# Kernel tuning notes

Hardware: AMD Instinct MI355X
Metric: run time of the kernel (lower is better)

## Reference

```python
import jax, jax.numpy as jnp
import numpy as np

DIM = 1024
HEADS = 16
HEAD_DIM = DIM // HEADS
MLP = 4 * DIM
EPS = 1e-5


def layer_norm(x, g, b):
    mu = jnp.mean(x, axis=-1, keepdims=True)
    var = jnp.var(x, axis=-1, keepdims=True)
    return (x - mu) * jax.lax.rsqrt(var + EPS) * g + b


def rope_cos_sin(n, d):
    inv_freq = 1.0 / (10000.0 ** (jnp.arange(0, d, 2, dtype=jnp.float32) / d))
    t = jnp.arange(n, dtype=jnp.float32)
    freqs = jnp.outer(t, inv_freq)          # [N, d/2]
    emb = jnp.concatenate([freqs, freqs], -1)  # [N, d]
    return jnp.cos(emb), jnp.sin(emb)


def rotate_half(x):
    x1, x2 = x[..., ::2], x[..., 1::2]
    return jnp.concatenate([-x2, x1], axis=-1)


def setup_inputs() -> dict:
    key = jax.random.key(0)
    ks = jax.random.split(key, 16)
    B, N = 2, 2048
    s = lambda fan_in: 1.0 / np.sqrt(fan_in)
    inp = {
        "x": jax.random.normal(ks[0], (B, N, DIM), jnp.float32),
        "t_emb": jax.random.normal(ks[1], (B, DIM), jnp.float32),
        "norm1_g": jnp.ones((DIM,), jnp.float32),
        "norm1_b": jnp.zeros((DIM,), jnp.float32),
        "Wq": jax.random.normal(ks[2], (DIM, DIM), jnp.float32) * s(DIM),
        "Wk": jax.random.normal(ks[3], (DIM, DIM), jnp.float32) * s(DIM),
        "Wv": jax.random.normal(ks[4], (DIM, DIM), jnp.float32) * s(DIM),
        "Wo": jax.random.normal(ks[5], (DIM, DIM), jnp.float32) * s(DIM),
        "norm2_g": jnp.ones((DIM,), jnp.float32),
        "norm2_b": jnp.zeros((DIM,), jnp.float32),
        "W1": jax.random.normal(ks[6], (DIM, MLP), jnp.float32) * s(DIM),
        "W2": jax.random.normal(ks[7], (MLP, DIM), jnp.float32) * s(MLP),
        "ada_W": jax.random.normal(ks[8], (DIM, 6 * DIM), jnp.float32) * s(DIM),
        "ada_b": jnp.zeros((6 * DIM,), jnp.float32),
    }
    return inp


def reference(x, t_emb, norm1_g, norm1_b, Wq, Wk, Wv, Wo,
              norm2_g, norm2_b, W1, W2, ada_W, ada_b):
    B, N, C = x.shape
    H, D = HEADS, HEAD_DIM
    scale = D ** -0.5

    mod = jax.nn.silu(t_emb) @ ada_W + ada_b          # [B, 6C]
    (shift_msa, scale_msa, gate_msa,
     shift_mlp, scale_mlp, gate_mlp) = jnp.split(mod, 6, axis=-1)

    xn = layer_norm(x, norm1_g, norm1_b) * (1 + scale_msa[:, None, :]) + shift_msa[:, None, :]

    q = (xn @ Wq).reshape(B, N, H, D).transpose(0, 2, 1, 3)  # [B,H,N,D]
    k = (xn @ Wk).reshape(B, N, H, D).transpose(0, 2, 1, 3)
    v = (xn @ Wv).reshape(B, N, H, D).transpose(0, 2, 1, 3)

    cos, sin = rope_cos_sin(N, D)                     # [N, D]
    q = q * cos + rotate_half(q) * sin
    k = k * cos + rotate_half(k) * sin

    attn = jnp.einsum('bhnd,bhmd->bhnm', q, k) * scale  # explicit O(N^2) scores
    attn = jax.nn.softmax(attn, axis=-1)
    out = jnp.einsum('bhnm,bhmd->bhnd', attn, v)

    out = out.transpose(0, 2, 1, 3).reshape(B, N, C) @ Wo
    x = x + gate_msa[:, None, :] * out

    xn = layer_norm(x, norm2_g, norm2_b) * (1 + scale_mlp[:, None, :]) + shift_mlp[:, None, :]
    mlp = jax.nn.gelu(xn @ W1, approximate=False) @ W2
    x = x + gate_mlp[:, None, :] * mlp
    return x
```

## Files before the change

kernel.cpp:

```cpp
#include <hip/hip_runtime.h>
#include <math.h>

#define BB    2
#define NN    2048
#define CDIM  1024
#define HEADS 16
#define HDIM  64
#define MLPD  4096
#define MODC  6144
#define EPSV  1e-5f
#define LOG2E 1.4426950408889634f
#define MSPLIT 16

typedef __attribute__((ext_vector_type(8))) short s8v;
typedef __attribute__((ext_vector_type(4))) float f4v;

__device__ inline unsigned short f2bf(float f) {
  union { float f; unsigned u; } v; v.f = f;
  unsigned r = v.u + 0x7FFFu + ((v.u >> 16) & 1u);
  return (unsigned short)(r >> 16);
}
__device__ inline float bf2f(unsigned short h) {
  union { unsigned u; float f; } v; v.u = ((unsigned)h) << 16;
  return v.f;
}

template<int CTRL>
__device__ __forceinline__ float dpp_max_step(float v) {
  int iv = __float_as_int(v);
  int sh = __builtin_amdgcn_update_dpp(iv, iv, CTRL, 0xF, 0xF, false);
  return fmaxf(v, __int_as_float(sh));
}
__device__ __forceinline__ float max16(float v) {
  v = dpp_max_step<0xB1>(v);
  v = dpp_max_step<0x4E>(v);
  v = dpp_max_step<0x124>(v);
  v = dpp_max_step<0x128>(v);
  return v;
}

__global__ __launch_bounds__(256) void mod_part(
    const float* __restrict__ t_emb, const float* __restrict__ ada_W,
    float* __restrict__ part) {
  int j = blockIdx.x * 256 + threadIdx.x;
  int b = blockIdx.y, ks = blockIdx.z;
  __shared__ float st[64];
  if (threadIdx.x < 64) {
    float v = t_emb[b * CDIM + ks * 64 + threadIdx.x];
    st[threadIdx.x] = v / (1.0f + expf(-v));
  }
  __syncthreads();
  float acc = 0.f;
  const float* wp = ada_W + (size_t)(ks * 64) * MODC + j;
  #pragma unroll 8
  for (int i = 0; i < 64; ++i) acc += st[i] * wp[(size_t)i * MODC];
  part[((size_t)ks * BB + b) * MODC + j] = acc;
}

__global__ __launch_bounds__(256) void mod_reduce(
    const float* __restrict__ part, const float* __restrict__ ada_b,
    float* __restrict__ mod) {
  int idx = blockIdx.x * 256 + threadIdx.x;
  int b = idx / MODC, j = idx % MODC;
  float a = ada_b[j];
  #pragma unroll
  for (int s = 0; s < MSPLIT; ++s) a += part[((size_t)s * BB + b) * MODC + j];
  mod[(size_t)b * MODC + j] = a;
}

__device__ inline float wave_sum64(float v) {
  for (int o = 32; o > 0; o >>= 1) v += __shfl_down(v, o, 64);
  return v;
}

__global__ __launch_bounds__(256) void ln_mod_bf16(
    const float* __restrict__ x, const float* __restrict__ g,
    const float* __restrict__ bta, const float* __restrict__ mod,
    int shift_off, int scale_off, unsigned short* __restrict__ out) {
  int r = blockIdx.x;
  int b = r / NN;
  int t = threadIdx.x;
  const float* xr = x + (size_t)r * CDIM;
  float4 xv = ((const float4*)xr)[t];
  float s  = xv.x + xv.y + xv.z + xv.w;
  float s2 = xv.x*xv.x + xv.y*xv.y + xv.z*xv.z + xv.w*xv.w;
  __shared__ float ws1[4], ws2[4];
  float sw = wave_sum64(s), s2w = wave_sum64(s2);
  int lane = t & 63, wid = t >> 6;
  if (lane == 0) { ws1[wid] = sw; ws2[wid] = s2w; }
  __syncthreads();
  float mu  = (ws1[0] + ws1[1] + ws1[2] + ws1[3]) * (1.0f / CDIM);
  float var = (ws2[0] + ws2[1] + ws2[2] + ws2[3]) * (1.0f / CDIM) - mu * mu;
  float rstd = rsqrtf(var + EPSV);
  const float* mods = mod + (size_t)b * MODC;
  float4 gv = ((const float4*)g)[t];
  float4 bv = ((const float4*)bta)[t];
  float4 sc = ((const float4*)(mods + scale_off))[t];
  float4 sh = ((const float4*)(mods + shift_off))[t];
  ushort4 ov;
  ov.x = f2bf(((xv.x - mu) * rstd * gv.x + bv.x) * (1.0f + sc.x) + sh.x);
  ov.y = f2bf(((xv.y - mu) * rstd * gv.y + bv.y) * (1.0f + sc.y) + sh.y);
  ov.z = f2bf(((xv.z - mu) * rstd * gv.z + bv.z) * (1.0f + sc.z) + sh.z);
  ov.w = f2bf(((xv.w - mu) * rstd * gv.w + bv.w) * (1.0f + sc.w) + sh.w);
  ((ushort4*)(out + (size_t)r * CDIM))[t] = ov;
}

__global__ __launch_bounds__(256) void wcast_all(
    const float* __restrict__ Wq, const float* __restrict__ Wk,
    const float* __restrict__ Wv, const float* __restrict__ Wo,
    const float* __restrict__ W1, const float* __restrict__ W2,
    unsigned short* __restrict__ Wqkvt, unsigned short* __restrict__ Wot,
    unsigned short* __restrict__ W1t, unsigned short* __restrict__ W2t) {
  int bid = blockIdx.x;
  const float* W; unsigned short* Wt; int K, N, t;
  if (bid < 4096) {
    int m = bid >> 10;
    t = bid & 1023;
    K = CDIM; N = CDIM;
    W  = (m == 0) ? Wq : (m == 1) ? Wk : (m == 2) ? Wv : Wo;
    Wt = (m == 3) ? Wot : (Wqkvt + (size_t)m * CDIM * CDIM);
  } else if (bid < 8192) {
    t = bid - 4096; K = CDIM; N = MLPD; W = W1; Wt = W1t;
  } else {
    t = bid - 8192; K = MLPD; N = CDIM; W = W2; Wt = W2t;
  }
  int ntiles = N >> 5;
  int n0 = (t % ntiles) * 32, k0 = (t / ntiles) * 32;
  __shared__ float tile[32][33];
  int tx = threadIdx.x & 31, ty = threadIdx.x >> 5;
  #pragma unroll
  for (int p = 0; p < 4; ++p)
    tile[ty + p * 8][tx] = W[(size_t)(k0 + ty + p * 8) * N + n0 + tx];
  __syncthreads();
  #pragma unroll
  for (int p = 0; p < 4; ++p)
    Wt[(size_t)(n0 + ty + p * 8) * K + k0 + tx] = f2bf(tile[tx][ty + p * 8]);
}

__global__ __launch_bounds__(1024) void mfma_gemm_big(
    const unsigned short* __restrict__ A,
    const unsigned short* __restrict__ Bt,
    int M, int N, int K,
    unsigned short* __restrict__ Ob, unsigned short* __restrict__ Ob2,
    unsigned short* __restrict__ Ob3, int mode) {
  __shared__ unsigned short SH[3 * 16384];
  int tid = threadIdx.x;
  int wave = tid >> 6, lane = tid & 63;
  int quad = lane >> 4, l15 = lane & 15;
  int m0 = blockIdx.y * 128, n0 = blockIdx.x * 128;
  int pos = wave & 7;
  int om = pos >> 1, on = pos & 1;
  int ks = wave >> 3;

  f4v acc[2][4] = {};

  int srow = lane >> 3;
  int ksrc = ((lane & 7) ^ (lane >> 3)) << 3;
  const int nt = K >> 6;

  #define STAGE_BIG(T, BUF)                                                    \
    {                                                                          \
      int k0_ = (T) << 6;                                                      \
      unsigned short* dsta = SH + (BUF) * 16384 + wave * 512;                  \
      const unsigned short* ga =                                               \
          A + (size_t)(m0 + 8 * wave + srow) * K + k0_ + ksrc;                 \
      __builtin_amdgcn_global_load_lds(                                        \
          (const __attribute__((address_space(1))) unsigned int*)(const void*)ga, \
          (__attribute__((address_space(3))) unsigned int*)(void*)dsta,        \
          16, 0, 0);                                                           \
      const unsigned short* gb =                                               \
          Bt + (size_t)(n0 + 8 * wave + srow) * K + k0_ + ksrc;                \
      __builtin_amdgcn_global_load_lds(                                        \
          (const __attribute__((address_space(1))) unsigned int*)(const void*)gb, \
          (__attribute__((address_space(3))) unsigned int*)(void*)(dsta + 8192), \
          16, 0, 0);                                                           \
    }

  STAGE_BIG(0, 0);
  STAGE_BIG(1, 1);
  asm volatile("s_waitcnt vmcnt(2)" ::: "memory");
  __syncthreads();

  int kx = (ks * 32 + quad * 8) ^ ((l15 & 7) << 3);

  int rbuf = 0, sbuf = 2;
  for (int t = 0; t < nt; ++t) {
    if (t + 2 < nt) STAGE_BIG(t + 2, sbuf);

    const unsigned short* base = SH + rbuf * 16384;
    s8v af[2], bf[4];
    #pragma unroll
    for (int i = 0; i < 2; ++i)
      af[i] = *(const s8v*)(base + (om * 32 + i * 16 + l15) * 64 + kx);
    #pragma unroll
    for (int j = 0; j < 4; ++j)
      bf[j] = *(const s8v*)(base + 8192 + (on * 64 + j * 16 + l15) * 64 + kx);
    #pragma unroll
    for (int i = 0; i < 2; ++i)
      #pragma unroll
      for (int j = 0; j < 4; ++j)
        acc[i][j] = __builtin_amdgcn_mfma_f32_16x16x32_bf16(
            af[i], bf[j], acc[i][j], 0, 0, 0);

    if (t + 2 < nt) {
      asm volatile("s_waitcnt vmcnt(2)" ::: "memory");
    } else if (t + 1 < nt) {
      asm volatile("s_waitcnt vmcnt(0)" ::: "memory");
    }
    __syncthreads();
    rbuf = (rbuf == 2) ? 0 : rbuf + 1;
    sbuf = (sbuf == 2) ? 0 : sbuf + 1;
  }
  #undef STAGE_BIG

  float* red = (float*)SH;
  if (wave >= 8) {
    int rb = (wave - 8) * 2304 + lane * 36;
    #pragma unroll
    for (int i = 0; i < 2; ++i)
      #pragma unroll
      for (int j = 0; j < 4; ++j)
        *(f4v*)(red + rb + (i * 4 + j) * 4) = acc[i][j];
  }
  __syncthreads();
  if (wave < 8) {
    int rb = wave * 2304 + lane * 36;
    #pragma unroll
    for (int i = 0; i < 2; ++i)
      #pragma unroll
      for (int j = 0; j < 4; ++j)
        acc[i][j] += *(const f4v*)(red + rb + (i * 4 + j) * 4);
    #pragma unroll
    for (int i = 0; i < 2; ++i) {
      int rbase = m0 + om * 32 + i * 16 + quad * 4;
      #pragma unroll
      for (int j = 0; j < 4; ++j) {
        int c = n0 + on * 64 + j * 16 + l15;
        #pragma unroll
        for (int rg = 0; rg < 4; ++rg) {
          int r = rbase + rg;
          float v = acc[i][j][rg];
          if (mode == 0) {
            unsigned short* dst = (c < 1024) ? Ob : ((c < 2048) ? Ob2 : Ob3);
            dst[(size_t)r * 1024 + (c & 1023)] = f2bf(v);
          } else {
            v = 0.5f * v * (1.0f + erff(v * 0.70710678118f));
            Ob[(size_t)r * N + c] = f2bf(v);
          }
        }
      }
    }
  }
}

__global__ __launch_bounds__(1024) void mfma_gemm_res(
    const unsigned short* __restrict__ A,
    const unsigned short* __restrict__ Bt,
    int M, int N, int K,
    float* __restrict__ O0,
    const float* __restrict__ res, const float* __restrict__ mod,
    int gate_off) {
  __shared__ unsigned short SH[3 * 16384];
  int tid = threadIdx.x;
  int wave = tid >> 6, lane = tid & 63;
  int quad = lane >> 4, l15 = lane & 15;
  int m0 = blockIdx.y * 128, n0 = blockIdx.x * 128;
  int pos = wave & 7;
  int om = pos >> 1, on = pos & 1;
  int ks = wave >> 3;

  f4v acc[2][4] = {};

  int srow = lane >> 3;
  int ksrc = ((lane & 7) ^ (lane >> 3)) << 3;
  const int nt = K >> 6;

  #define STAGE_RES(T, BUF)                                                    \
    {                                                                          \
      int k0_ = (T) << 6;                                                      \
      unsigned short* dsta = SH + (BUF) * 16384 + wave * 512;                  \
      const unsigned short* ga =                                               \
          A + (size_t)(m0 + 8 * wave + srow) * K + k0_ + ksrc;                 \
      __builtin_amdgcn_global_load_lds(                                        \
          (const __attribute__((address_space(1))) unsigned int*)(const void*)ga, \
          (__attribute__((address_space(3))) unsigned int*)(void*)dsta,        \
          16, 0, 0);                                                           \
      const unsigned short* gb =                                               \
          Bt + (size_t)(n0 + 8 * wave + srow) * K + k0_ + ksrc;                \
      __builtin_amdgcn_global_load_lds(                                        \
          (const __attribute__((address_space(1))) unsigned int*)(const void*)gb, \
          (__attribute__((address_space(3))) unsigned int*)(void*)(dsta + 8192), \
          16, 0, 0);                                                           \
    }

  STAGE_RES(0, 0);
  STAGE_RES(1, 1);
  asm volatile("s_waitcnt vmcnt(2)" ::: "memory");
  __syncthreads();

  int kx = (ks * 32 + quad * 8) ^ ((l15 & 7) << 3);

  int rbuf = 0, sbuf = 2;
  for (int t = 0; t < nt; ++t) {
    if (t + 2 < nt) STAGE_RES(t + 2, sbuf);

    const unsigned short* base = SH + rbuf * 16384;
    s8v af[2], bf[4];
    #pragma unroll
    for (int i = 0; i < 2; ++i)
      af[i] = *(const s8v*)(base + (om * 32 + i * 16 + l15) * 64 + kx);
    #pragma unroll
    for (int j = 0; j < 4; ++j)
      bf[j] = *(const s8v*)(base + 8192 + (on * 64 + j * 16 + l15) * 64 + kx);
    #pragma unroll
    for (int i = 0; i < 2; ++i)
      #pragma unroll
      for (int j = 0; j < 4; ++j)
        acc[i][j] = __builtin_amdgcn_mfma_f32_16x16x32_bf16(
            af[i], bf[j], acc[i][j], 0, 0, 0);

    if (t + 2 < nt) {
      asm volatile("s_waitcnt vmcnt(2)" ::: "memory");
    } else if (t + 1 < nt) {
      asm volatile("s_waitcnt vmcnt(0)" ::: "memory");
    }
    __syncthreads();
    rbuf = (rbuf == 2) ? 0 : rbuf + 1;
    sbuf = (sbuf == 2) ? 0 : sbuf + 1;
  }
  #undef STAGE_RES

  float* red = (float*)SH;
  if (wave >= 8) {
    int rb = (wave - 8) * 2304 + lane * 36;
    #pragma unroll
    for (int i = 0; i < 2; ++i)
      #pragma unroll
      for (int j = 0; j < 4; ++j)
        *(f4v*)(red + rb + (i * 4 + j) * 4) = acc[i][j];
  }
  __syncthreads();
  if (wave < 8) {
    int rb = wave * 2304 + lane * 36;
    #pragma unroll
    for (int i = 0; i < 2; ++i)
      #pragma unroll
      for (int j = 0; j < 4; ++j)
        acc[i][j] += *(const f4v*)(red + rb + (i * 4 + j) * 4);
    #pragma unroll
    for (int i = 0; i < 2; ++i) {
      int rbase = m0 + om * 32 + i * 16 + quad * 4;
      #pragma unroll
      for (int j = 0; j < 4; ++j) {
        int c = n0 + on * 64 + j * 16 + l15;
        #pragma unroll
        for (int rg = 0; rg < 4; ++rg) {
          int r = rbase + rg;
          int bb2 = r >> 11;
          O0[(size_t)r * N + c] =
              res[(size_t)r * N + c] + mod[bb2 * MODC + gate_off + c] * acc[i][j][rg];
        }
      }
    }
  }
}

__global__ __launch_bounds__(256) void rope_qk(
    unsigned short* __restrict__ qb, const unsigned short* __restrict__ kb,
    unsigned short* __restrict__ kpack, float qscale) {
  int r = blockIdx.x;
  int b = r / NN, n = r % NN;
  int t = threadIdx.x;
  int isK = blockIdx.y;
  const unsigned short* src = isK ? kb : qb;
  float scale = isK ? 1.0f : qscale;
  __shared__ float row[CDIM];
  __shared__ float csv[32], snv[32];
  if (t < 32) {
    float invf = powf(10000.0f, -(float)t / 32.0f);
    float sn, cs;
    sincosf((float)n * invf, &sn, &cs);
    csv[t] = cs * scale; snv[t] = sn * scale;
  }
  const unsigned short* qr = src + (size_t)r * CDIM;
  ushort4 xv = ((const ushort4*)qr)[t];
  row[t * 4 + 0] = bf2f(xv.x);
  row[t * 4 + 1] = bf2f(xv.y);
  row[t * 4 + 2] = bf2f(xv.z);
  row[t * 4 + 3] = bf2f(xv.w);
  __syncthreads();
  unsigned short o[4];
  int c0 = t * 4;
  #pragma unroll
  for (int q4 = 0; q4 < 4; ++q4) {
    int c = c0 + q4;
    int h = c >> 6, d = c & 63;
    int i = d & 31;
    float rh = (d < 32) ? -row[h * 64 + 2 * d + 1] : row[h * 64 + 2 * (d - 32)];
    o[q4] = f2bf(row[c] * csv[i] + rh * snv[i]);
  }
  if (!isK) {
    ((ushort4*)(qb + (size_t)r * CDIM))[t] = make_ushort4(o[0], o[1], o[2], o[3]);
  } else {
    int h = c0 >> 6, d0 = c0 & 63;
    int half = d0 >> 5, quad = (d0 >> 3) & 3, j0 = d0 & 7;
    int bh = b * HEADS + h;
    int tt = n >> 6, kt = (n >> 4) & 3, l15 = n & 15;
    int lane = quad * 16 + l15;
    size_t off = ((((size_t)bh * 32 + tt) * 8 + kt * 2 + half) * 64 + lane) * 8 + j0;
    unsigned int lo = (unsigned)o[0] | ((unsigned)o[1] << 16);
    unsigned int hi = (unsigned)o[2] | ((unsigned)o[3] << 16);
    *(uint2*)(kpack + off) = make_uint2(lo, hi);
  }
}

__global__ __launch_bounds__(256) void vtrans_pack(
    const unsigned short* __restrict__ vrow, unsigned short* __restrict__ vpack) {
  int t = blockIdx.x;
  int bh = blockIdx.y;
  int b = bh >> 4, h = bh & 15;
  __shared__ unsigned short L[64 * 72];
  int tid = threadIdx.x;
  #pragma unroll
  for (int p = 0; p < 2; ++p) {
    int c = tid + p * 256;
    int key = c >> 3, dc = (c & 7) * 8;
    *(s8v*)(L + key * 72 + dc) =
        *(const s8v*)(vrow + (size_t)(b * NN + t * 64 + key) * CDIM + h * HDIM + dc);
  }
  __syncthreads();
  #pragma unroll
  for (int p = 0; p < 2; ++p) {
    int o = tid + p * 256;
    int f = o >> 6, lane = o & 63;
    int dt = f >> 1, half = f & 1, quad = lane >> 4, l15 = lane & 15;
    int d = dt * 16 + l15;
    unsigned short tmp[8];
    #pragma unroll
    for (int j = 0; j < 8; ++j) {
      int key = (j & 3) * 16 + half * 8 + quad * 2 + (j >> 2);
      tmp[j] = L[key * 72 + d];
    }
    *(s8v*)(vpack + ((((size_t)bh * 32 + t) * 8 + f) * 64 + lane) * 8) = *(s8v*)tmp;
  }
}

__global__ __launch_bounds__(512) void fattn_pack(
    const unsigned short* __restrict__ qb,
    const unsigned short* __restrict__ kpack,
    const unsigned short* __restrict__ vpack,
    unsigned short* __restrict__ ob) {
  int bid = blockIdx.x;
  int qt = bid >> 5, bh = bid & 31;
  int b = bh >> 4, h = bh & 15;
  int tid = threadIdx.x;
  int wave = tid >> 6, lane = tid & 63;
  int quad = lane >> 4, l15 = lane & 15;

  __shared__ unsigned short smem[3 * 8192 + 8 * 2304];
  unsigned short* Pw = smem + 3 * 8192 + wave * 2304;

  int n0 = qt * 256;
  s8v qf[2][2];
  #pragma unroll
  for (int fq = 0; fq < 2; ++fq) {
    int qrow = n0 + wave * 32 + fq * 16 + l15;
    const unsigned short* qp = qb + (size_t)(b * NN + qrow) * CDIM + h * HDIM;
    qf[fq][0] = *(const s8v*)(qp + quad * 8);
    qf[fq][1] = *(const s8v*)(qp + 32 + quad * 8);
  }

  f4v acc[2][4] = {};
  float m_i[2][4], l_i[2][4];
  #pragma unroll
  for (int fq = 0; fq < 2; ++fq)
    #pragma unroll
    for (int r = 0; r < 4; ++r) { m_i[fq][r] = -1e30f; l_i[fq][r] = 0.f; }

  const unsigned short* ksrc = kpack + (size_t)bh * 131072 + wave * 512 + lane * 8;
  const unsigned short* vsrc = vpack + (size_t)bh * 131072 + wave * 512 + lane * 8;

  #define STAGE_ATT(T, BUF)                                                    \
    {                                                                          \
      __builtin_amdgcn_global_load_lds(                                        \
          (const __attribute__((address_space(1))) unsigned int*)(const void*)(ksrc + (size_t)(T) * 4096), \
          (__attribute__((address_space(3))) unsigned int*)(void*)(smem + (BUF) * 8192 + wave * 512), \
          16, 0, 0);                                                           \
      __builtin_amdgcn_global_load_lds(                                        \
          (const __attribute__((address_space(1))) unsigned int*)(const void*)(vsrc + (size_t)(T) * 4096), \
          (__attribute__((address_space(3))) unsigned int*)(void*)(smem + (BUF) * 8192 + 4096 + wave * 512), \
          16, 0, 0);                                                           \
    }

  const int NT = NN / 64;
  STAGE_ATT(0, 0);
  STAGE_ATT(1, 1);
  asm volatile("s_waitcnt vmcnt(2)" ::: "memory");
  __syncthreads();

  int rbuf = 0, sbuf = 2;
  for (int t = 0; t < NT; ++t) {
    if (t + 2 < NT) STAGE_ATT(t + 2, sbuf);

    const unsigned short* kb_ = smem + rbuf * 8192 + lane * 8;
    f4v s4[2][4];
    {
      s8v kf[8];
      #pragma unroll
      for (int f = 0; f < 8; ++f) kf[f] = *(const s8v*)(kb_ + f * 512);
      #pragma unroll
      for (int fq = 0; fq < 2; ++fq)
        #pragma unroll
        for (int kt = 0; kt < 4; ++kt) {
          f4v z = {};
          z = __builtin_amdgcn_mfma_f32_16x16x32_bf16(qf[fq][0], kf[kt * 2], z, 0, 0, 0);
          z = __builtin_amdgcn_mfma_f32_16x16x32_bf16(qf[fq][1], kf[kt * 2 + 1], z, 0, 0, 0);
          s4[fq][kt] = z;
        }
    }

    #pragma unroll
    for (int fq = 0; fq < 2; ++fq)
      #pragma unroll
      for (int r = 0; r < 4; ++r) {
        float mv = fmaxf(fmaxf(s4[fq][0][r], s4[fq][1][r]),
                         fmaxf(s4[fq][2][r], s4[fq][3][r]));
        mv = max16(mv);
        if (!__all(mv - m_i[fq][r] <= 8.0f)) {
          float mnew = fmaxf(m_i[fq][r], mv);
          float alpha = __builtin_amdgcn_exp2f(m_i[fq][r] - mnew);
          m_i[fq][r] = mnew;
          l_i[fq][r] *= alpha;
          acc[fq][0][r] *= alpha; acc[fq][1][r] *= alpha;
          acc[fq][2][r] *= alpha; acc[fq][3][r] *= alpha;
        }
        float ls = 0.f;
        #pragma unroll
        for (int kt = 0; kt < 4; ++kt) {
          float p = __builtin_amdgcn_exp2f(s4[fq][kt][r] - m_i[fq][r]);
          s4[fq][kt][r] = p;
          ls += p;
        }
        l_i[fq][r] += ls;
      }

    #pragma unroll
    for (int fq = 0; fq < 2; ++fq)
      #pragma unroll
      for (int r = 0; r < 4; ++r) {
        unsigned int lo = (__float_as_uint(s4[fq][0][r]) >> 16) |
                          (__float_as_uint(s4[fq][1][r]) & 0xffff0000u);
        unsigned int hi = (__float_as_uint(s4[fq][2][r]) >> 16) |
                          (__float_as_uint(s4[fq][3][r]) & 0xffff0000u);
        *(uint2*)(Pw + (fq * 16 + quad * 4 + r) * 72 + l15 * 4) = make_uint2(lo, hi);
      }

    {
      const unsigned short* vb_ = smem + rbuf * 8192 + 4096 + lane * 8;
      s8v vf[8];
      #pragma unroll
      for (int f = 0; f < 8; ++f) vf[f] = *(const s8v*)(vb_ + f * 512);
      #pragma unroll
      for (int fq = 0; fq < 2; ++fq) {
        s8v pf0 = *(const s8v*)(Pw + (fq * 16 + l15) * 72 + quad * 8);
        s8v pf1 = *(const s8v*)(Pw + (fq * 16 + l15) * 72 + 32 + quad * 8);
        #pragma unroll
        for (int dt = 0; dt < 4; ++dt) {
          acc[fq][dt] = __builtin_amdgcn_mfma_f32_16x16x32_bf16(pf0, vf[dt * 2], acc[fq][dt], 0, 0, 0);
          acc[fq][dt] = __builtin_amdgcn_mfma_f32_16x16x32_bf16(pf1, vf[dt * 2 + 1], acc[fq][dt], 0, 0, 0);
        }
      }
    }

    if (t + 2 < NT) {
      asm volatile("s_waitcnt vmcnt(2)" ::: "memory");
    } else if (t + 1 < NT) {
      asm volatile("s_waitcnt vmcnt(0)" ::: "memory");
    }
    __syncthreads();
    rbuf = (rbuf == 2) ? 0 : rbuf + 1;
    sbuf = (sbuf == 2) ? 0 : sbuf + 1;
  }
  #undef STAGE_ATT

  #pragma unroll
  for (int fq = 0; fq < 2; ++fq)
    #pragma unroll
    for (int r = 0; r < 4; ++r) {
      float l = l_i[fq][r];
      #pragma unroll
      for (int msk = 1; msk < 16; msk <<= 1)
        l += __shfl_xor(l, msk, 64);
      float inv = 1.0f / l;
      size_t row = (size_t)(b * NN + n0 + wave * 32 + fq * 16 + quad * 4 + r);
      unsigned short* op = ob + row * CDIM + h * HDIM;
      #pragma unroll
      for (int dt = 0; dt < 4; ++dt)
        op[dt * 16 + l15] = f2bf(acc[fq][dt][r] * inv);
    }
}

extern "C" void kernel_launch(void* const* d_in, const int* in_sizes, int n_in,
                              void* d_out, int out_size, void* d_ws, size_t ws_size,
                              hipStream_t stream) {
  const float* x    = (const float*)d_in[0];
  const float* temb = (const float*)d_in[1];
  const float* n1g  = (const float*)d_in[2];
  const float* n1b  = (const float*)d_in[3];
  const float* Wq   = (const float*)d_in[4];
  const float* Wk   = (const float*)d_in[5];
  const float* Wv   = (const float*)d_in[6];
  const float* Wo   = (const float*)d_in[7];
  const float* n2g  = (const float*)d_in[8];
  const float* n2b  = (const float*)d_in[9];
  const float* W1   = (const float*)d_in[10];
  const float* W2   = (const float*)d_in[11];
  const float* adaW = (const float*)d_in[12];
  const float* adab = (const float*)d_in[13];
  float* out = (float*)d_out;

  const size_t TOK = (size_t)BB * NN * CDIM;
  float* wsf = (float*)d_ws;
  float* mod     = wsf;
  float* modpart = wsf + 16384;
  unsigned short* tokb  = (unsigned short*)(wsf + 16384 + MSPLIT * BB * MODC);
  unsigned short* qb    = tokb + TOK;
  unsigned short* kb    = qb + TOK;
  unsigned short* kpack = kb + TOK;
  unsigned short* vpack = kpack + TOK;
  unsigned short* Wqkvt = vpack + TOK;
  unsigned short* Wot   = Wqkvt + 3 * CDIM * CDIM;
  unsigned short* W1t   = Wot + CDIM * CDIM;
  unsigned short* W2t   = W1t + CDIM * MLPD;
  unsigned short* h1b   = W2t + MLPD * CDIM;
  unsigned short* vrow  = h1b;
  float* x1 = (float*)qb;

  const int M = BB * NN;

  mod_part<<<dim3(MODC / 256, BB, MSPLIT), 256, 0, stream>>>(temb, adaW, modpart);
  mod_reduce<<<dim3(BB * MODC / 256), 256, 0, stream>>>(modpart, adab, mod);
  ln_mod_bf16<<<dim3(M), 256, 0, stream>>>(x, n1g, n1b, mod, 0, 1024, tokb);

  wcast_all<<<dim3(12288), 256, 0, stream>>>(
      Wq, Wk, Wv, Wo, W1, W2, Wqkvt, Wot, W1t, W2t);

  mfma_gemm_big<<<dim3(24, 32), 1024, 0, stream>>>(
      tokb, Wqkvt, M, 3 * CDIM, CDIM, qb, kb, vrow, 0);

  rope_qk<<<dim3(M, 2), 256, 0, stream>>>(qb, kb, kpack, 0.125f * LOG2E);

  vtrans_pack<<<dim3(NN / 64, BB * HEADS), 256, 0, stream>>>(vrow, vpack);

  fattn_pack<<<dim3((NN / 256) * BB * HEADS), 512, 0, stream>>>(
      qb, kpack, vpack, tokb);

  mfma_gemm_res<<<dim3(CDIM / 128, M / 128), 1024, 0, stream>>>(
      tokb, Wot, M, CDIM, CDIM, x1, x, mod, 2048);

  ln_mod_bf16<<<dim3(M), 256, 0, stream>>>(x1, n2g, n2b, mod, 3072, 4096, tokb);

  mfma_gemm_big<<<dim3(MLPD / 128, M / 128), 1024, 0, stream>>>(
      tokb, W1t, M, MLPD, CDIM, h1b, nullptr, nullptr, 1);

  mfma_gemm_res<<<dim3(CDIM / 128, M / 128), 1024, 0, stream>>>(
      h1b, W2t, M, CDIM, MLPD, out, x1, mod, 5120);
}
```

Measured before the change: 422.8 us.

## Use 256x256 output tiles with 16 waves for QKV and W1 GEMMs

Replaces the 128x128 split-K GEMM, where 16 waves split K in two and reduce through LDS, with a 256x256 tile. Each of the 16 waves now owns a 64x64 output block over the full K, double-buffered instead of triple-buffered. This doubles operand reuse per LDS load and removes the split-K reduction. The cost is more accumulator registers per wave and fewer blocks: 192 for QKV and 256 for W1 on a 256-CU part, so occupancy and load balance get worse.

```diff
diff --git a/kernel.cpp b/kernel.cpp
--- a/kernel.cpp
+++ b/kernel.cpp
@@ -137,116 +137,98 @@
     Wt[(size_t)(n0 + ty + p * 8) * K + k0 + tx] = f2bf(tile[tx][ty + p * 8]);
 }
 
-__global__ __launch_bounds__(1024) void mfma_gemm_big(
+__global__ __launch_bounds__(1024) void mfma_gemm_256(
     const unsigned short* __restrict__ A,
     const unsigned short* __restrict__ Bt,
     int M, int N, int K,
     unsigned short* __restrict__ Ob, unsigned short* __restrict__ Ob2,
     unsigned short* __restrict__ Ob3, int mode) {
-  __shared__ unsigned short SH[3 * 16384];
+  __shared__ unsigned short SH[2 * 32768];
   int tid = threadIdx.x;
   int wave = tid >> 6, lane = tid & 63;
   int quad = lane >> 4, l15 = lane & 15;
-  int m0 = blockIdx.y * 128, n0 = blockIdx.x * 128;
-  int pos = wave & 7;
-  int om = pos >> 1, on = pos & 1;
-  int ks = wave >> 3;
-
-  f4v acc[2][4] = {};
+  int m0 = blockIdx.y * 256, n0 = blockIdx.x * 256;
+  int wr = wave >> 2, wc = wave & 3;
+
+  f4v acc[4][4] = {};
 
   int srow = lane >> 3;
   int ksrc = ((lane & 7) ^ (lane >> 3)) << 3;
   const int nt = K >> 6;
 
-  #define STAGE_BIG(T, BUF)                                                    \
+  #define STAGE_256(T, BUF)                                                    \
     {                                                                          \
       int k0_ = (T) << 6;                                                      \
-      unsigned short* dsta = SH + (BUF) * 16384 + wave * 512;                  \
-      const unsigned short* ga =                                               \
-          A + (size_t)(m0 + 8 * wave + srow) * K + k0_ + ksrc;                 \
-      __builtin_amdgcn_global_load_lds(                                        \
-          (const __attribute__((address_space(1))) unsigned int*)(const void*)ga, \
-          (__attribute__((address_space(3))) unsigned int*)(void*)dsta,        \
-          16, 0, 0);                                                           \
-      const unsigned short* gb =                                               \
-          Bt + (size_t)(n0 + 8 * wave + srow) * K + k0_ + ksrc;                \
-      __builtin_amdgcn_global_load_lds(                                        \
-          (const __attribute__((address_space(1))) unsigned int*)(const void*)gb, \
-          (__attribute__((address_space(3))) unsigned int*)(void*)(dsta + 8192), \
-          16, 0, 0);                                                           \
-    }
-
-  STAGE_BIG(0, 0);
-  STAGE_BIG(1, 1);
-  asm volatile("s_waitcnt vmcnt(2)" ::: "memory");
-  __syncthreads();
-
-  int kx = (ks * 32 + quad * 8) ^ ((l15 & 7) << 3);
-
-  int rbuf = 0, sbuf = 2;
+      unsigned short* ab = SH + (BUF) * 32768 + wave * 1024;                   \
+      _Pragma("unroll")                                                        \
+      for (int s = 0; s < 2; ++s) {                                            \
+        const unsigned short* ga =                                             \
+            A + (size_t)(m0 + 16 * wave + 8 * s + srow) * K + k0_ + ksrc;      \
+        __builtin_amdgcn_global_load_lds(                                      \
+            (const __attribute__((address_space(1))) unsigned int*)(const void*)ga, \
+            (__attribute__((address_space(3))) unsigned int*)(void*)(ab + s * 512), \
+            16, 0, 0);                                                         \
+        const unsigned short* gb =                                             \
+            Bt + (size_t)(n0 + 16 * wave + 8 * s + srow) * K + k0_ + ksrc;     \
+        __builtin_amdgcn_global_load_lds(                                      \
+            (const __attribute__((address_space(1))) unsigned int*)(const void*)gb, \
+            (__attribute__((address_space(3))) unsigned int*)(void*)(ab + 16384 + s * 512), \
+            16, 0, 0);                                                         \
+      }                                                                        \
+    }
+
+  STAGE_256(0, 0);
+  asm volatile("s_waitcnt vmcnt(0)" ::: "memory");
+  __syncthreads();
+
+  int buf = 0;
   for (int t = 0; t < nt; ++t) {
-    if (t + 2 < nt) STAGE_BIG(t + 2, sbuf);
-
-    const unsigned short* base = SH + rbuf * 16384;
-    s8v af[2], bf[4];
-    #pragma unroll
-    for (int i = 0; i < 2; ++i)
-      af[i] = *(const s8v*)(base + (om * 32 + i * 16 + l15) * 64 + kx);
-    #pragma unroll
-    for (int j = 0; j < 4; ++j)
-      bf[j] = *(const s8v*)(base + 8192 + (on * 64 + j * 16 + l15) * 64 + kx);
-    #pragma unroll
-    for (int i = 0; i < 2; ++i)
+    if (t + 1 < nt) STAGE_256(t + 1, buf ^ 1);
+
+    const unsigned short* Ab = SH + buf * 32768;
+    const unsigned short* Bb = Ab + 16384;
+    #pragma unroll
+    for (int ks = 0; ks < 2; ++ks) {
+      int kx = (ks * 32 + quad * 8) ^ ((l15 & 7) << 3);
+      s8v af[4], bf[4];
+      #pragma unroll
+      for (int i = 0; i < 4; ++i)
+        af[i] = *(const s8v*)(Ab + (wr * 64 + i * 16 + l15) * 64 + kx);
       #pragma unroll
       for (int j = 0; j < 4; ++j)
-        acc[i][j] = __builtin_amdgcn_mfma_f32_16x16x32_bf16(
-            af[i], bf[j], acc[i][j], 0, 0, 0);
-
-    if (t + 2 < nt) {
-      asm volatile("s_waitcnt vmcnt(2)" ::: "memory");
-    } else if (t + 1 < nt) {
+        bf[j] = *(const s8v*)(Bb + (wc * 64 + j * 16 + l15) * 64 + kx);
+      #pragma unroll
+      for (int i = 0; i < 4; ++i)
+        #pragma unroll
+        for (int j = 0; j < 4; ++j)
+          acc[i][j] = __builtin_amdgcn_mfma_f32_16x16x32_bf16(
+              af[i], bf[j], acc[i][j], 0, 0, 0);
+    }
+
+    if (t + 1 < nt) {
       asm volatile("s_waitcnt vmcnt(0)" ::: "memory");
-    }
-    __syncthreads();
-    rbuf = (rbuf == 2) ? 0 : rbuf + 1;
-    sbuf = (sbuf == 2) ? 0 : sbuf + 1;
-  }
-  #undef STAGE_BIG
-
-  float* red = (float*)SH;
-  if (wave >= 8) {
-    int rb = (wave - 8) * 2304 + lane * 36;
-    #pragma unroll
-    for (int i = 0; i < 2; ++i)
-      #pragma unroll
-      for (int j = 0; j < 4; ++j)
-        *(f4v*)(red + rb + (i * 4 + j) * 4) = acc[i][j];
-  }
-  __syncthreads();
-  if (wave < 8) {
-    int rb = wave * 2304 + lane * 36;
-    #pragma unroll
-    for (int i = 0; i < 2; ++i)
-      #pragma unroll
-      for (int j = 0; j < 4; ++j)
-        acc[i][j] += *(const f4v*)(red + rb + (i * 4 + j) * 4);
-    #pragma unroll
-    for (int i = 0; i < 2; ++i) {
-      int rbase = m0 + om * 32 + i * 16 + quad * 4;
-      #pragma unroll
-      for (int j = 0; j < 4; ++j) {
-        int c = n0 + on * 64 + j * 16 + l15;
-        #pragma unroll
-        for (int rg = 0; rg < 4; ++rg) {
-          int r = rbase + rg;
-          float v = acc[i][j][rg];
-          if (mode == 0) {
-            unsigned short* dst = (c < 1024) ? Ob : ((c < 2048) ? Ob2 : Ob3);
-            dst[(size_t)r * 1024 + (c & 1023)] = f2bf(v);
-          } else {
-            v = 0.5f * v * (1.0f + erff(v * 0.70710678118f));
-            Ob[(size_t)r * N + c] = f2bf(v);
-          }
+      __syncthreads();
+      buf ^= 1;
+    }
+  }
+  #undef STAGE_256
+
+  #pragma unroll
+  for (int i = 0; i < 4; ++i) {
+    int rbase = m0 + wr * 64 + i * 16 + quad * 4;
+    #pragma unroll
+    for (int j = 0; j < 4; ++j) {
+      int c = n0 + wc * 64 + j * 16 + l15;
+      #pragma unroll
+      for (int rg = 0; rg < 4; ++rg) {
+        int r = rbase + rg;
+        float v = acc[i][j][rg];
+        if (mode == 0) {
+          unsigned short* dst = (c < 1024) ? Ob : ((c < 2048) ? Ob2 : Ob3);
+          dst[(size_t)r * 1024 + (c & 1023)] = f2bf(v);
+        } else {
+          v = 0.5f * v * (1.0f + erff(v * 0.70710678118f));
+          Ob[(size_t)r * N + c] = f2bf(v);
         }
       }
     }
@@ -645,7 +627,7 @@
   wcast_all<<<dim3(12288), 256, 0, stream>>>(
       Wq, Wk, Wv, Wo, W1, W2, Wqkvt, Wot, W1t, W2t);
 
-  mfma_gemm_big<<<dim3(24, 32), 1024, 0, stream>>>(
+  mfma_gemm_256<<<dim3(3 * CDIM / 256, M / 256), 1024, 0, stream>>>(
       tokb, Wqkvt, M, 3 * CDIM, CDIM, qb, kb, vrow, 0);
 
   rope_qk<<<dim3(M, 2), 256, 0, stream>>>(qb, kb, kpack, 0.125f * LOG2E);
@@ -660,7 +642,7 @@
 
   ln_mod_bf16<<<dim3(M), 256, 0, stream>>>(x1, n2g, n2b, mod, 3072, 4096, tokb);
 
-  mfma_gemm_big<<<dim3(MLPD / 128, M / 128), 1024, 0, stream>>>(
+  mfma_gemm_256<<<dim3(MLPD / 256, M / 256), 1024, 0, stream>>>(
       tokb, W1t, M, MLPD, CDIM, h1b, nullptr, nullptr, 1);
 
   mfma_gemm_res<<<dim3(CDIM / 128, M / 128), 1024, 0, stream>>>(
```

Result: faster. 389.1 us, median of 2 (-8.0%).
